# Performance work log

Measured on AMD Instinct MI355X. Metric: run time of the kernel, lower is better.

The kernel has to match this reference:

```python
import jax, jax.numpy as jnp
import numpy as np

H = 512        # hidden_dim
D_IN = 512     # input_dim
N_ACT = 16     # output_dim
DICT = 8192    # dict_len (episodic memory slots)
B = 4096       # batch
N_CYCLES = 10  # LCA iterations
DT_T = 0.6     # LCA dt/tau
EPS = 1e-8     # cosine-similarity eps


def setup_inputs() -> dict:
    key = jax.random.key(0)
    ks = jax.random.split(key, 12)
    NHT = 4 * H + 3  # (N_VSIG+1)*H + N_SSIG
    s = lambda i, shape, sc=1.0: jax.random.normal(ks[i], shape, jnp.float32) * sc
    return {
        "x_t": s(0, (1, B, D_IN)),
        "h_prev": s(1, (1, B, H), 0.1),
        "c_prev": s(2, (1, B, H), 0.1),
        "W_i2h": s(3, (NHT, D_IN), 1.0 / np.sqrt(D_IN)),
        "b_i2h": jnp.zeros((NHT,), jnp.float32),
        "W_h2h": s(4, (NHT, H), 1.0 / np.sqrt(H)),
        "b_h2h": jnp.zeros((NHT,), jnp.float32),
        "vals": s(5, (DICT, H), 0.1),  # episodic memory table
        "W_ih": s(6, (H, H), 1.0 / np.sqrt(H)),
        "b_ih": jnp.zeros((H,), jnp.float32),
        "W_actor": s(7, (N_ACT, H), 1.0 / np.sqrt(H)),
        "b_actor": jnp.zeros((N_ACT,), jnp.float32),
        "W_critic": s(8, (1, H), 1.0 / np.sqrt(H)),
        "b_critic": jnp.zeros((1,), jnp.float32),
        "mem_ptr": 0,
    }


def _lca(sim, leak, comp, w_input):
    # Leaky competing accumulator over memory slots; sim:[B,DICT], scalars:[B,1]
    ff = w_input * sim
    def step(V, _):
        inhib = comp * (jnp.sum(V, axis=-1, keepdims=True) - V)  # lateral inhibition (excl. self)
        V = jax.nn.relu(V + DT_T * (ff - leak * V - inhib))
        return V, None
    V, _ = jax.lax.scan(step, jnp.zeros_like(sim), None, length=N_CYCLES)
    return V


def reference(x_t, h_prev, c_prev, W_i2h, b_i2h, W_h2h, b_h2h, vals,
              W_ih, b_ih, W_actor, b_actor, W_critic, b_critic, mem_ptr):
    x, h, c = x_t[0], h_prev[0], c_prev[0]  # [B, dim]
    preact = x @ W_i2h.T + b_i2h + h @ W_h2h.T + b_h2h  # [B, 4H+3]
    gates = jax.nn.sigmoid(preact[:, :3 * H])
    f_t = gates[:, :H]
    o_t = gates[:, H:2 * H]
    i_t = gates[:, 2 * H:3 * H]
    inps = jax.nn.sigmoid(preact[:, 3 * H + 0])[:, None]  # input strength (gain=1)
    leak = jax.nn.sigmoid(preact[:, 3 * H + 1])[:, None]
    comp = jax.nn.sigmoid(preact[:, 3 * H + 2])[:, None]
    c_new = jnp.tanh(preact[:, 3 * H + 3:])
    c_t = c * f_t + i_t * c_new
    # --- recall: cosine similarity vs memory, then LCA competition ---
    qn = jnp.linalg.norm(c_t, axis=-1, keepdims=True)        # [B,1]
    mn = jnp.linalg.norm(vals, axis=-1, keepdims=True)       # [DICT,1]
    sim = (c_t @ vals.T) / jnp.maximum(qn * mn.T, EPS)       # [B,DICT]
    w = _lca(sim, leak, comp, inps)                          # [B,DICT]
    m_t = w @ vals                                           # [B,H]
    cm_t = c_t + m_t
    # --- encode: ring-buffer scatter write of cm_t into memory ---
    idx = (mem_ptr + jnp.arange(B)) % DICT
    new_vals = vals.at[idx].set(cm_t)
    h_t = o_t * jnp.tanh(cm_t)
    # --- A2C head ---
    a2c_h = jax.nn.relu(h_t @ W_ih.T + b_ih)
    pi = jax.nn.softmax(a2c_h @ W_actor.T + b_actor, axis=-1)
    value = a2c_h @ W_critic.T + b_critic
    return pi, value, h_t, cm_t, m_t, new_vals
```

## Files before the change

kernel.cpp:

```cpp
#include <hip/hip_runtime.h>
#include <hip/hip_fp16.h>
#include <math.h>

#define HH    512
#define DICT  8192
#define BATCH 4096
#define NCYC  10
#define DTT   0.6f

#define BM  128
#define BKT 64

using f16x8 = __attribute__((ext_vector_type(8))) _Float16;
using f32x4 = __attribute__((ext_vector_type(4))) float;

__device__ __forceinline__ float sigmoidf_(float x) { return 1.0f / (1.0f + __expf(-x)); }

__device__ __forceinline__ float waveReduceSum(float v) {
#pragma unroll
  for (int o = 1; o < 64; o <<= 1) v += __shfl_xor(v, o);
  return v;
}

__device__ __forceinline__ void gld16(const void* g, void* l) {
  __builtin_amdgcn_global_load_lds(
      (const __attribute__((address_space(1))) void*)g,
      (__attribute__((address_space(3))) void*)l, 16, 0, 0);
}

template<int N> __device__ __forceinline__ void vmwait() {
  if constexpr (N == 8)      asm volatile("s_waitcnt vmcnt(8)" ::: "memory");
  else if constexpr (N == 6) asm volatile("s_waitcnt vmcnt(6)" ::: "memory");
  else                       asm volatile("s_waitcnt vmcnt(0)" ::: "memory");
  __builtin_amdgcn_sched_barrier(0);
}

__device__ __forceinline__ void blockbar() {
  asm volatile("" ::: "memory");
  __builtin_amdgcn_s_barrier();
  __builtin_amdgcn_sched_barrier(0);
}

template<int ROWS>
__device__ __forceinline__ void stage_tile(const __half* gbase, int ld, char* lds, int tid) {
  constexpr int ISS = ROWS * 8 / 256;
#pragma unroll
  for (int i = 0; i < ISS; ++i) {
    int cidx = i * 256 + tid;
    int row  = cidx >> 3;
    int slot = cidx & 7;
    int k4   = slot ^ (row & 7);
    gld16(gbase + (size_t)row * ld + k4 * 8, lds + cidx * 16);
  }
}

__device__ __forceinline__ f16x8 frag_ld(const char* lds, int row, int kchunk) {
  int slot = kchunk ^ (row & 7);
  return *(const f16x8*)(lds + row * 128 + slot * 16);
}

template<int FN>
__device__ __forceinline__ void tile_mfma(const char* As, const char* Bs,
                                          int lane, int wr, int wc, f32x4 (&acc)[4][FN]) {
  const int g = lane >> 4, r = lane & 15;
#pragma unroll
  for (int ks = 0; ks < 2; ++ks) {
    f16x8 af[4], bfr[FN];
#pragma unroll
    for (int i = 0; i < 4; ++i)
      af[i] = frag_ld(As, wr * 64 + i * 16 + r, ks * 4 + g);
#pragma unroll
    for (int j = 0; j < FN; ++j)
      bfr[j] = frag_ld(Bs, wc * (FN * 16) + j * 16 + r, ks * 4 + g);
#pragma unroll
    for (int i = 0; i < 4; ++i)
#pragma unroll
      for (int j = 0; j < FN; ++j)
        acc[i][j] = __builtin_amdgcn_mfma_f32_16x16x32_f16(af[i], bfr[j], acc[i][j], 0, 0, 0);
  }
}

template<int BN, int FN>
__device__ __forceinline__ void gemm_seg(const __half* A, int lda, const __half* B, int ldb,
                                         int m0, int n0, int K, char* lds, int tid,
                                         f32x4 (&acc)[4][FN]) {
  constexpr int ABYTES = BM * BKT * 2;
  constexpr int BBYTES = BN * BKT * 2;
  constexpr int BUF = ABYTES + BBYTES;
  constexpr int NL = (BM + BN) * 8 / 256;
  const int lane = tid & 63, wid = tid >> 6;
  const int wr = wid >> 1, wc = wid & 1;
  const int nt = K / BKT;
  const __half* Ab = A + (size_t)m0 * lda;
  const __half* Bb = B + (size_t)n0 * ldb;
  stage_tile<BM>(Ab, lda, lds, tid);
  stage_tile<BN>(Bb, ldb, lds + ABYTES, tid);
  int cur = 0;
  for (int t = 0; t < nt; ++t) {
    char* curb = lds + cur * BUF;
    if (t + 1 < nt) {
      char* nxt = lds + (cur ^ 1) * BUF;
      stage_tile<BM>(Ab + (t + 1) * BKT, lda, nxt, tid);
      stage_tile<BN>(Bb + (t + 1) * BKT, ldb, nxt + ABYTES, tid);
      vmwait<NL>();
    } else {
      vmwait<0>();
    }
    blockbar();
    tile_mfma<FN>(curb, curb + ABYTES, lane, wr, wc, acc);
    blockbar();
    cur ^= 1;
  }
}

__device__ __forceinline__ void zero_acc4(f32x4 (&a)[4][4]) {
  f32x4 z = {0.f, 0.f, 0.f, 0.f};
#pragma unroll
  for (int i = 0; i < 4; ++i)
#pragma unroll
    for (int j = 0; j < 4; ++j) a[i][j] = z;
}
__device__ __forceinline__ void zero_acc2(f32x4 (&a)[4][2]) {
  f32x4 z = {0.f, 0.f, 0.f, 0.f};
#pragma unroll
  for (int i = 0; i < 4; ++i)
#pragma unroll
    for (int j = 0; j < 2; ++j) a[i][j] = z;
}

__global__ __launch_bounds__(256) void k_prep(
    const float* __restrict__ x, const float* __restrict__ h,
    const float* __restrict__ Wi, const float* __restrict__ Wh, const float* __restrict__ Wih,
    const float* __restrict__ vals, const int* __restrict__ mptr,
    __half* __restrict__ x_h, __half* __restrict__ h_h,
    __half* __restrict__ Wip_h, __half* __restrict__ Whp_h, __half* __restrict__ Wih_h,
    float* __restrict__ nv, __half* __restrict__ vals_h, float* __restrict__ rmn,
    __half* __restrict__ vT) {
  __shared__ float tile[32][33];
  const int bid = blockIdx.x;
  if (bid < 6400) {
    int gq = bid * 256 + threadIdx.x;
    const float* src; __half* dst; int si, di;
    if (gq < 524288) {
      src = x; dst = x_h; si = di = gq * 4;
    } else if (gq < 1048576) {
      src = h; dst = h_h; si = di = (gq - 524288) * 4;
    } else if (gq < 1310720) {
      int iq = gq - 1048576;
      int jp = iq >> 7, k4 = (iq & 127) << 2;
      int U = jp >> 6, g = (jp >> 4) & 3, r = jp & 15;
      int u = U * 16 + r;
      int orig = g * 512 + u + (g == 3 ? 3 : 0);
      src = Wi; dst = Wip_h; si = orig * 512 + k4; di = jp * 512 + k4;
    } else if (gq < 1572864) {
      int iq = gq - 1310720;
      int jp = iq >> 7, k4 = (iq & 127) << 2;
      int U = jp >> 6, g = (jp >> 4) & 3, r = jp & 15;
      int u = U * 16 + r;
      int orig = g * 512 + u + (g == 3 ? 3 : 0);
      src = Wh; dst = Whp_h; si = orig * 512 + k4; di = jp * 512 + k4;
    } else if (gq < 1638400) {
      int iq = gq - 1572864;
      src = Wih; dst = Wih_h; si = di = iq * 4;
    } else return;
    float4 v = *(const float4*)(src + si);
    *(__half2*)(dst + di)     = __floats2half2_rn(v.x, v.y);
    *(__half2*)(dst + di + 2) = __floats2half2_rn(v.z, v.w);
  } else if (bid < 8448) {
    const int row  = (bid - 6400) * 4 + (threadIdx.x >> 6);
    const int lane = threadIdx.x & 63;
    const float* vr = vals + (size_t)row * HH + lane * 8;
    float4 a = *(const float4*)(vr);
    float4 b = *(const float4*)(vr + 4);
    if (((row + DICT - mptr[0]) & (DICT - 1)) >= BATCH) {
      float* nvp = nv + (size_t)row * HH + lane * 8;
      *(float4*)(nvp)     = a;
      *(float4*)(nvp + 4) = b;
    }
    __half* vh = vals_h + (size_t)row * HH + lane * 8;
    *(__half2*)(vh)     = __floats2half2_rn(a.x, a.y);
    *(__half2*)(vh + 2) = __floats2half2_rn(a.z, a.w);
    *(__half2*)(vh + 4) = __floats2half2_rn(b.x, b.y);
    *(__half2*)(vh + 6) = __floats2half2_rn(b.z, b.w);
    float ss = a.x * a.x + a.y * a.y + a.z * a.z + a.w * a.w
             + b.x * b.x + b.y * b.y + b.z * b.z + b.w * b.w;
    ss = waveReduceSum(ss);
    if (lane == 0) rmn[row] = 1.f / fmaxf(sqrtf(ss), 1e-12f);
  } else {
    const int idx = bid - 8448;
    const int r0 = (idx & 255) * 32, c0 = (idx >> 8) * 32;
    const int tr = threadIdx.x >> 5, tc = threadIdx.x & 31;
#pragma unroll
    for (int p = 0; p < 4; ++p)
      tile[tr + p * 8][tc] = vals[(size_t)(r0 + tr + p * 8) * HH + c0 + tc];
    __syncthreads();
#pragma unroll
    for (int p = 0; p < 4; ++p)
      vT[(size_t)(c0 + tr + p * 8) * DICT + r0 + tc] = __float2half(tile[tc][tr + p * 8]);
  }
}

__global__ __launch_bounds__(256) void k_preact(
    const __half* __restrict__ x_h, const __half* __restrict__ h_h,
    const __half* __restrict__ Wip, const __half* __restrict__ Whp,
    const float* __restrict__ bi, const float* __restrict__ bh,
    const float* __restrict__ c_prev,
    float* __restrict__ ct, float* __restrict__ ot, __half* __restrict__ ct_h) {
  __shared__ char smem[2 * (BM * BKT * 2 + 128 * BKT * 2)] __attribute__((aligned(16)));
  const int tid = threadIdx.x;
  const int m0 = blockIdx.y * 128, n0 = blockIdx.x * 128;
  f32x4 acc[4][4]; zero_acc4(acc);
  gemm_seg<128, 4>(x_h, HH, Wip, HH, m0, n0, HH, smem, tid, acc);
  gemm_seg<128, 4>(h_h, HH, Whp, HH, m0, n0, HH, smem, tid, acc);
  const int lane = tid & 63, wid = tid >> 6, wr = wid >> 1, wc = wid & 1;
  const int r = lane & 15;
  const int u = ((n0 >> 6) + wc) * 16 + r;
  float bsum[4];
#pragma unroll
  for (int g = 0; g < 4; ++g) {
    int orig = g * 512 + u + (g == 3 ? 3 : 0);
    bsum[g] = bi[orig] + bh[orig];
  }
#pragma unroll
  for (int fi = 0; fi < 4; ++fi)
#pragma unroll
    for (int q = 0; q < 4; ++q) {
      int m = m0 + wr * 64 + fi * 16 + (lane >> 4) * 4 + q;
      float f  = sigmoidf_(acc[fi][0][q] + bsum[0]);
      float o  = sigmoidf_(acc[fi][1][q] + bsum[1]);
      float ii = sigmoidf_(acc[fi][2][q] + bsum[2]);
      float cn = tanhf(acc[fi][3][q] + bsum[3]);
      size_t off = (size_t)m * HH + u;
      float cc = c_prev[off] * f + ii * cn;
      ct[off] = cc; ot[off] = o; ct_h[off] = __float2half(cc);
    }
}

__global__ __launch_bounds__(256) void k_scalars(
    const float* __restrict__ x, const float* __restrict__ h,
    const float* __restrict__ Wi, const float* __restrict__ Wh,
    const float* __restrict__ bi, const float* __restrict__ bh,
    const float* __restrict__ ct,
    float* __restrict__ inps, float* __restrict__ leak,
    float* __restrict__ comp, float* __restrict__ rqn) {
  const int b = blockIdx.x, wid = threadIdx.x >> 6, lane = threadIdx.x & 63;
  const int j = lane * 8;
  if (wid < 3) {
    const float* wi = Wi + (size_t)(1536 + wid) * HH + j;
    const float* wh = Wh + (size_t)(1536 + wid) * HH + j;
    const float* xr = x + (size_t)b * HH + j;
    const float* hr = h + (size_t)b * HH + j;
    float4 xa = *(const float4*)(xr), xb = *(const float4*)(xr + 4);
    float4 wa = *(const float4*)(wi), wb = *(const float4*)(wi + 4);
    float4 ha = *(const float4*)(hr), hb = *(const float4*)(hr + 4);
    float4 va = *(const float4*)(wh), vb = *(const float4*)(wh + 4);
    float s = xa.x * wa.x + xa.y * wa.y + xa.z * wa.z + xa.w * wa.w
            + xb.x * wb.x + xb.y * wb.y + xb.z * wb.z + xb.w * wb.w
            + ha.x * va.x + ha.y * va.y + ha.z * va.z + ha.w * va.w
            + hb.x * vb.x + hb.y * vb.y + hb.z * vb.z + hb.w * vb.w;
    s = waveReduceSum(s);
    if (lane == 0) {
      float v = sigmoidf_(s + bi[1536 + wid] + bh[1536 + wid]);
      if (wid == 0) inps[b] = v; else if (wid == 1) leak[b] = v; else comp[b] = v;
    }
  } else {
    const float* cr = ct + (size_t)b * HH + j;
    float4 a = *(const float4*)(cr), d = *(const float4*)(cr + 4);
    float ss = a.x * a.x + a.y * a.y + a.z * a.z + a.w * a.w
             + d.x * d.x + d.y * d.y + d.z * d.z + d.w * d.w;
    ss = waveReduceSum(ss);
    if (lane == 0) rqn[b] = 1.f / fmaxf(sqrtf(ss), 1e-12f);
  }
}

__global__ __launch_bounds__(256) void k_sim(
    const __half* __restrict__ ct_h, const __half* __restrict__ vals_h,
    const float* __restrict__ rqn, const float* __restrict__ rmn,
    __half* __restrict__ sim_h) {
  __shared__ char smem[2 * (BM * BKT * 2 + 128 * BKT * 2)] __attribute__((aligned(16)));
  const int tid = threadIdx.x;
  const int m0 = blockIdx.y * 128, n0 = blockIdx.x * 128;
  f32x4 acc[4][4]; zero_acc4(acc);
  gemm_seg<128, 4>(ct_h, HH, vals_h, HH, m0, n0, HH, smem, tid, acc);
  const int lane = tid & 63, wid = tid >> 6, wr = wid >> 1, wc = wid & 1;
  float* T = (float*)smem;
  const int g = lane >> 4, r = lane & 15;
  const int lrow = tid >> 3, c16 = (tid & 7) * 16;
  const int nR = n0 + c16;
  float rmv[16];
  *(float4*)(rmv)      = *(const float4*)(rmn + nR);
  *(float4*)(rmv + 4)  = *(const float4*)(rmn + nR + 4);
  *(float4*)(rmv + 8)  = *(const float4*)(rmn + nR + 8);
  *(float4*)(rmv + 12) = *(const float4*)(rmn + nR + 12);
#pragma unroll
  for (int fi = 0; fi < 4; ++fi) {
    if (fi) __syncthreads();
#pragma unroll
    for (int fj = 0; fj < 4; ++fj)
#pragma unroll
      for (int q = 0; q < 4; ++q)
        T[(wr * 16 + g * 4 + q) * 132 + wc * 64 + fj * 16 + r] = acc[fi][fj][q];
    __syncthreads();
    int m = m0 + (lrow >> 4) * 64 + fi * 16 + (lrow & 15);
    float rq = rqn[m];
    const float* Tr = T + lrow * 132 + c16;
    f16x8 o0, o1;
#pragma unroll
    for (int j = 0; j < 8; ++j) o0[j] = (_Float16)(Tr[j] * rq * rmv[j]);
#pragma unroll
    for (int j = 0; j < 8; ++j) o1[j] = (_Float16)(Tr[8 + j] * rq * rmv[8 + j]);
    *(f16x8*)(sim_h + (size_t)m * DICT + nR)     = o0;
    *(f16x8*)(sim_h + (size_t)m * DICT + nR + 8) = o1;
  }
}

__global__ __launch_bounds__(256) void k_lca(
    const __half* __restrict__ sim_h, const float* __restrict__ inps,
    const float* __restrict__ leak, const float* __restrict__ comp,
    __half* __restrict__ w_h) {
  const int b = blockIdx.x, t = threadIdx.x;
  const __half* srow = sim_h + (size_t)b * DICT + t * 32;
  const float ffs = DTT * inps[b];
  const float a   = 1.0f - DTT * leak[b] + DTT * comp[b];
  const float cdt = DTT * comp[b];
  float ff[32], V[32];
#pragma unroll
  for (int i = 0; i < 4; ++i) {
    f16x8 v8 = *(const f16x8*)(srow + i * 8);
#pragma unroll
    for (int j = 0; j < 8; ++j) { ff[i * 8 + j] = ffs * (float)v8[j]; V[i * 8 + j] = 0.f; }
  }
  __shared__ float ps[4];
  for (int it = 0; it < NCYC; ++it) {
    float s = 0.f;
#pragma unroll
    for (int i = 0; i < 32; ++i) s += V[i];
    s = waveReduceSum(s);
    if ((t & 63) == 0) ps[t >> 6] = s;
    __syncthreads();
    float S = ps[0] + ps[1] + ps[2] + ps[3];
    __syncthreads();
    float sub = cdt * S;
#pragma unroll
    for (int i = 0; i < 32; ++i) V[i] = fmaxf(fmaf(a, V[i], ff[i] - sub), 0.f);
  }
  __half* wrow = w_h + (size_t)b * DICT + t * 32;
#pragma unroll
  for (int i = 0; i < 4; ++i) {
    f16x8 o8;
#pragma unroll
    for (int j = 0; j < 8; ++j) o8[j] = (_Float16)V[i * 8 + j];
    *(f16x8*)(wrow + i * 8) = o8;
  }
}

__global__ __launch_bounds__(256) void k_mt_p(
    const __half* __restrict__ w_h, const __half* __restrict__ vT_h,
    float* __restrict__ partial) {
  __shared__ char smem[2 * (BM * BKT * 2 + 64 * BKT * 2)] __attribute__((aligned(16)));
  const int tid = threadIdx.x, bid = blockIdx.x;
  const int xcd = bid & 7, idx = bid >> 3;
  const int n = idx & 7, q = idx >> 3;
  const int g = (q << 3) | xcd;
  const int m = g >> 2, s = g & 3;
  const int m0 = m * 128, n0 = n * 64;
  f32x4 acc[4][2]; zero_acc2(acc);
  gemm_seg<64, 2>(w_h + s * 2048, DICT, vT_h + s * 2048, DICT, m0, n0, 2048, smem, tid, acc);
  const int lane = tid & 63, wid = tid >> 6, wr = wid >> 1, wc = wid & 1;
  float* pbase = partial + (size_t)s * (BATCH * HH);
  float* T = (float*)smem;
  const int gg = lane >> 4, r = lane & 15;
  const int lrow = tid >> 3, c8 = (tid & 7) * 8;
#pragma unroll
  for (int fi = 0; fi < 4; ++fi) {
    if (fi) __syncthreads();
#pragma unroll
    for (int fj = 0; fj < 2; ++fj)
#pragma unroll
      for (int qq = 0; qq < 4; ++qq)
        T[(wr * 16 + gg * 4 + qq) * 68 + wc * 32 + fj * 16 + r] = acc[fi][fj][qq];
    __syncthreads();
    int mm = m0 + (lrow >> 4) * 64 + fi * 16 + (lrow & 15);
    float* dst = pbase + (size_t)mm * HH + n0 + c8;
    *(float4*)dst       = *(const float4*)(T + lrow * 68 + c8);
    *(float4*)(dst + 4) = *(const float4*)(T + lrow * 68 + c8 + 4);
  }
}

__global__ __launch_bounds__(256) void k_mt_red(
    const float* __restrict__ partial,
    const float* __restrict__ ct, const float* __restrict__ ot, const int* __restrict__ mptr,
    float* __restrict__ out_mt, float* __restrict__ out_cmt, float* __restrict__ out_ht,
    float* __restrict__ out_nv, __half* __restrict__ ht_h) {
  const int i4 = blockIdx.x * 256 + threadIdx.x;
  const size_t off = (size_t)i4 * 4;
  const int m = i4 >> 7;
  float4 p  = *(const float4*)(partial + off);
  float4 p1 = *(const float4*)(partial + 2097152 + off);
  float4 p2 = *(const float4*)(partial + 4194304 + off);
  float4 p3 = *(const float4*)(partial + 6291456 + off);
  p.x += p1.x + p2.x + p3.x;
  p.y += p1.y + p2.y + p3.y;
  p.z += p1.z + p2.z + p3.z;
  p.w += p1.w + p2.w + p3.w;
  float4 c4 = *(const float4*)(ct + off);
  float4 o4 = *(const float4*)(ot + off);
  float4 cm, hv;
  cm.x = c4.x + p.x; hv.x = o4.x * tanhf(cm.x);
  cm.y = c4.y + p.y; hv.y = o4.y * tanhf(cm.y);
  cm.z = c4.z + p.z; hv.z = o4.z * tanhf(cm.z);
  cm.w = c4.w + p.w; hv.w = o4.w * tanhf(cm.w);
  *(float4*)(out_mt + off)  = p;
  *(float4*)(out_cmt + off) = cm;
  *(float4*)(out_ht + off)  = hv;
  *(__half2*)(ht_h + off)     = __floats2half2_rn(hv.x, hv.y);
  *(__half2*)(ht_h + off + 2) = __floats2half2_rn(hv.z, hv.w);
  const int nvrow = (mptr[0] + m) & (DICT - 1);
  *(float4*)(out_nv + (size_t)nvrow * HH + (off & 511)) = cm;
}

__global__ __launch_bounds__(256) void k_a2c(
    const __half* __restrict__ ht_h, const __half* __restrict__ Wih_h,
    const float* __restrict__ bih, float* __restrict__ a2c) {
  __shared__ char smem[2 * (BM * BKT * 2 + 64 * BKT * 2)] __attribute__((aligned(16)));
  const int tid = threadIdx.x;
  const int bid = blockIdx.x;
  const int xn = (bid >> 3) & 7, ym = (bid & 7) | ((bid >> 6) << 3);
  const int m0 = ym * 128, n0 = xn * 64;
  f32x4 acc[4][2]; zero_acc2(acc);
  gemm_seg<64, 2>(ht_h, HH, Wih_h, HH, m0, n0, HH, smem, tid, acc);
  const int lane = tid & 63, wid = tid >> 6, wr = wid >> 1, wc = wid & 1;
  float* T = (float*)smem;
  const int gg = lane >> 4, r = lane & 15;
  const int lrow = tid >> 3, c8 = (tid & 7) * 8;
  float4 b0 = *(const float4*)(bih + n0 + c8);
  float4 b1 = *(const float4*)(bih + n0 + c8 + 4);
#pragma unroll
  for (int fi = 0; fi < 4; ++fi) {
    if (fi) __syncthreads();
#pragma unroll
    for (int fj = 0; fj < 2; ++fj)
#pragma unroll
      for (int qq = 0; qq < 4; ++qq)
        T[(wr * 16 + gg * 4 + qq) * 68 + wc * 32 + fj * 16 + r] = acc[fi][fj][qq];
    __syncthreads();
    int mm = m0 + (lrow >> 4) * 64 + fi * 16 + (lrow & 15);
    float4 v0 = *(const float4*)(T + lrow * 68 + c8);
    float4 v1 = *(const float4*)(T + lrow * 68 + c8 + 4);
    v0.x = fmaxf(v0.x + b0.x, 0.f); v0.y = fmaxf(v0.y + b0.y, 0.f);
    v0.z = fmaxf(v0.z + b0.z, 0.f); v0.w = fmaxf(v0.w + b0.w, 0.f);
    v1.x = fmaxf(v1.x + b1.x, 0.f); v1.y = fmaxf(v1.y + b1.y, 0.f);
    v1.z = fmaxf(v1.z + b1.z, 0.f); v1.w = fmaxf(v1.w + b1.w, 0.f);
    float* dst = a2c + (size_t)mm * HH + n0 + c8;
    *(float4*)dst       = v0;
    *(float4*)(dst + 4) = v1;
  }
}

__global__ __launch_bounds__(256) void k_actor(
    const float* __restrict__ a2c,
    const float* __restrict__ Wact, const float* __restrict__ bact,
    const float* __restrict__ Wcr, const float* __restrict__ bcr,
    float* __restrict__ out_pi, float* __restrict__ out_val) {
  const int b = blockIdx.x * 4 + (threadIdx.x >> 6);
  const int lane = threadIdx.x & 63;
  const float* hrow = a2c + (size_t)b * HH;
  float4 a0 = *(const float4*)(hrow + (lane << 3));
  float4 a1 = *(const float4*)(hrow + (lane << 3) + 4);
  float lg[17];
#pragma unroll
  for (int o = 0; o < 17; ++o) {
    const float* wr = (o < 16) ? (Wact + (size_t)o * HH) : Wcr;
    float4 w0 = *(const float4*)(wr + (lane << 3));
    float4 w1 = *(const float4*)(wr + (lane << 3) + 4);
    float s = a0.x * w0.x + a0.y * w0.y + a0.z * w0.z + a0.w * w0.w
            + a1.x * w1.x + a1.y * w1.y + a1.z * w1.z + a1.w * w1.w;
    lg[o] = waveReduceSum(s);
  }
#pragma unroll
  for (int o = 0; o < 16; ++o) lg[o] += bact[o];
  float mx = lg[0];
#pragma unroll
  for (int o = 1; o < 16; ++o) mx = fmaxf(mx, lg[o]);
  float e[16], sum = 0.f;
#pragma unroll
  for (int o = 0; o < 16; ++o) { e[o] = __expf(lg[o] - mx); sum += e[o]; }
  float rs = 1.f / sum;
  if (lane == 0) {
#pragma unroll
    for (int o = 0; o < 16; ++o) out_pi[(size_t)b * 16 + o] = e[o] * rs;
    out_val[b] = lg[16] + bcr[0];
  }
}

extern "C" void kernel_launch(void* const* d_in, const int* in_sizes, int n_in,
                              void* d_out, int out_size, void* d_ws, size_t ws_size,
                              hipStream_t stream) {
  const float* x    = (const float*)d_in[0];
  const float* h    = (const float*)d_in[1];
  const float* c    = (const float*)d_in[2];
  const float* Wi   = (const float*)d_in[3];
  const float* bi   = (const float*)d_in[4];
  const float* Wh   = (const float*)d_in[5];
  const float* bh   = (const float*)d_in[6];
  const float* vals = (const float*)d_in[7];
  const float* Wih  = (const float*)d_in[8];
  const float* bih  = (const float*)d_in[9];
  const float* Wact = (const float*)d_in[10];
  const float* bact = (const float*)d_in[11];
  const float* Wcr  = (const float*)d_in[12];
  const float* bcr  = (const float*)d_in[13];
  const int*   mptr = (const int*)d_in[14];

  float* F = (float*)d_ws;
  __half* w_h    = (__half*)F;
  __half* sim_h   = (__half*)(F + 16777216);
  float*  a2c     = F + 16777216;
  float*  partial = F + 33554432;
  float*  ct     = F + 50331648;
  float*  ot     = F + 52428800;
  __half* ct_h   = (__half*)(F + 54525952);
  __half* vals_h = (__half*)(F + 55574528);
  __half* vT_h   = (__half*)(F + 57671680);
  __half* x_h    = (__half*)(F + 59768832);
  __half* ht_h   = x_h;
  __half* h_h    = (__half*)(F + 60817408);
  __half* Wip_h  = (__half*)(F + 61865984);
  __half* Whp_h  = (__half*)(F + 62423040);
  __half* Wih_h  = (__half*)(F + 62980096);
  float*  inps   = F + 63111168;
  float*  leak   = inps + 4096;
  float*  comp   = leak + 4096;
  float*  rqn    = comp + 4096;
  float*  rmn    = rqn + 4096;

  float* out     = (float*)d_out;
  float* out_pi  = out;
  float* out_val = out + 65536;
  float* out_ht  = out + 69632;
  float* out_cmt = out_ht + 2097152;
  float* out_mt  = out_cmt + 2097152;
  float* out_nv  = out_mt + 2097152;

  dim3 b256(256);
  k_prep   <<<12544, b256, 0, stream>>>(x, h, Wi, Wh, Wih, vals, mptr,
                                        x_h, h_h, Wip_h, Whp_h, Wih_h,
                                        out_nv, vals_h, rmn, vT_h);
  k_preact <<<dim3(16, 32), b256, 0, stream>>>(x_h, h_h, Wip_h, Whp_h, bi, bh, c,
                                               ct, ot, ct_h);
  k_scalars<<<BATCH, b256, 0, stream>>>(x, h, Wi, Wh, bi, bh, ct, inps, leak, comp, rqn);
  k_sim    <<<dim3(64, 32), b256, 0, stream>>>(ct_h, vals_h, rqn, rmn, sim_h);
  k_lca    <<<BATCH, b256, 0, stream>>>(sim_h, inps, leak, comp, w_h);
  k_mt_p   <<<1024, b256, 0, stream>>>(w_h, vT_h, partial);
  k_mt_red <<<2048, b256, 0, stream>>>(partial, ct, ot, mptr,
                                       out_mt, out_cmt, out_ht, out_nv, ht_h);
  k_a2c    <<<256, b256, 0, stream>>>(ht_h, Wih_h, bih, a2c);
  k_actor  <<<BATCH / 4, b256, 0, stream>>>(a2c, Wact, bact, Wcr, bcr, out_pi, out_val);
}
```

Baseline: 218.7 us.

## Enlarge sim and mt GEMM tiles with 512-thread blocks and XCD-aware mapping

Rewrites the two large GEMMs (similarity and memory readout) to use 256x256 and 256x128 tiles with 512-thread blocks, K-step 32 using the 16x16x32 f16 MFMA, XOR-swizzled LDS staging and double buffering with finer vmcnt waits. Block indices are remapped so that blocks sharing an A row tile land on the same XCD, for L2 reuse. The aim is higher arithmetic intensity and less redundant global traffic. In exchange the kernels carry more accumulator registers and launch fewer blocks (512 and 256), which risks low occupancy or wave-quantization tail effects.

Measured after the change: 235.9 us. 1.08x slower.

```diff
diff --git a/kernel.cpp b/kernel.cpp
--- a/kernel.cpp
+++ b/kernel.cpp
@@ -31,6 +31,8 @@
 template<int N> __device__ __forceinline__ void vmwait() {
   if constexpr (N == 8)      asm volatile("s_waitcnt vmcnt(8)" ::: "memory");
   else if constexpr (N == 6) asm volatile("s_waitcnt vmcnt(6)" ::: "memory");
+  else if constexpr (N == 4) asm volatile("s_waitcnt vmcnt(4)" ::: "memory");
+  else if constexpr (N == 3) asm volatile("s_waitcnt vmcnt(3)" ::: "memory");
   else                       asm volatile("s_waitcnt vmcnt(0)" ::: "memory");
   __builtin_amdgcn_sched_barrier(0);
 }
@@ -126,6 +128,45 @@
   for (int i = 0; i < 4; ++i)
 #pragma unroll
     for (int j = 0; j < 2; ++j) a[i][j] = z;
+}
+
+__device__ __forceinline__ int swz32(int row, int k) {
+  return k ^ (row & 3) ^ ((row >> 2) & 3);
+}
+
+template<int ROWS, int NT>
+__device__ __forceinline__ void stage32(const __half* gbase, int ld, char* lds, int tid) {
+  constexpr int ISS = ROWS * 4 / NT;
+#pragma unroll
+  for (int i = 0; i < ISS; ++i) {
+    int cidx = i * NT + tid;
+    int row  = cidx >> 2;
+    int slot = cidx & 3;
+    int k4   = swz32(row, slot);
+    gld16(gbase + (size_t)row * ld + k4 * 8, lds + cidx * 16);
+  }
+}
+
+__device__ __forceinline__ f16x8 frag32(const char* lds, int row, int g) {
+  int slot = swz32(row, g);
+  return *(const f16x8*)(lds + row * 64 + slot * 16);
+}
+
+template<int MF, int NF>
+__device__ __forceinline__ void tile_mfma32(const char* As, const char* Bs,
+                                            int arow0, int brow0, int lane,
+                                            f32x4 (&acc)[MF][NF]) {
+  const int g = lane >> 4, r = lane & 15;
+  f16x8 af[MF], bf[NF];
+#pragma unroll
+  for (int i = 0; i < MF; ++i) af[i] = frag32(As, arow0 + i * 16 + r, g);
+#pragma unroll
+  for (int j = 0; j < NF; ++j) bf[j] = frag32(Bs, brow0 + j * 16 + r, g);
+#pragma unroll
+  for (int i = 0; i < MF; ++i)
+#pragma unroll
+    for (int j = 0; j < NF; ++j)
+      acc[i][j] = __builtin_amdgcn_mfma_f32_16x16x32_f16(af[i], bf[j], acc[i][j], 0, 0, 0);
 }
 
 __global__ __launch_bounds__(256) void k_prep(
@@ -273,44 +314,72 @@
   }
 }
 
-__global__ __launch_bounds__(256) void k_sim(
+__global__ __launch_bounds__(512, 2) void k_sim(
     const __half* __restrict__ ct_h, const __half* __restrict__ vals_h,
     const float* __restrict__ rqn, const float* __restrict__ rmn,
     __half* __restrict__ sim_h) {
-  __shared__ char smem[2 * (BM * BKT * 2 + 128 * BKT * 2)] __attribute__((aligned(16)));
-  const int tid = threadIdx.x;
-  const int m0 = blockIdx.y * 128, n0 = blockIdx.x * 128;
-  f32x4 acc[4][4]; zero_acc4(acc);
-  gemm_seg<128, 4>(ct_h, HH, vals_h, HH, m0, n0, HH, smem, tid, acc);
-  const int lane = tid & 63, wid = tid >> 6, wr = wid >> 1, wc = wid & 1;
+  __shared__ char smem[65536] __attribute__((aligned(16)));
+  const int tid = threadIdx.x, lane = tid & 63, wid = tid >> 6;
+  const int wr = wid >> 2, wc = wid & 3;
+  const int bid = blockIdx.x;
+  const int xcd = bid & 7, idx = bid >> 3;
+  const int m0 = (xcd * 2 + (idx & 1)) * 256;
+  const int n0 = (idx >> 1) * 256;
+  f32x4 acc[8][4];
+  { f32x4 z = {0.f, 0.f, 0.f, 0.f};
+#pragma unroll
+    for (int i = 0; i < 8; ++i)
+#pragma unroll
+      for (int j = 0; j < 4; ++j) acc[i][j] = z; }
+  const __half* Ab = ct_h + (size_t)m0 * HH;
+  const __half* Bb = vals_h + (size_t)n0 * HH;
+  stage32<256, 512>(Ab, HH, smem, tid);
+  stage32<256, 512>(Bb, HH, smem + 16384, tid);
+  int cur = 0;
+  for (int t = 0; t < 16; ++t) {
+    char* curb = smem + cur * 32768;
+    if (t < 15) {
+      char* nxt = smem + (cur ^ 1) * 32768;
+      stage32<256, 512>(Ab + (t + 1) * 32, HH, nxt, tid);
+      stage32<256, 512>(Bb + (t + 1) * 32, HH, nxt + 16384, tid);
+      vmwait<4>();
+    } else {
+      vmwait<0>();
+    }
+    blockbar();
+    __builtin_amdgcn_s_setprio(1);
+    tile_mfma32<8, 4>(curb, curb + 16384, wr * 128, wc * 64, lane, acc);
+    __builtin_amdgcn_s_setprio(0);
+    blockbar();
+    cur ^= 1;
+  }
   float* T = (float*)smem;
   const int g = lane >> 4, r = lane & 15;
-  const int lrow = tid >> 3, c16 = (tid & 7) * 16;
-  const int nR = n0 + c16;
+  const int lrow = tid >> 4, seg = (tid & 15) * 16;
   float rmv[16];
-  *(float4*)(rmv)      = *(const float4*)(rmn + nR);
-  *(float4*)(rmv + 4)  = *(const float4*)(rmn + nR + 4);
-  *(float4*)(rmv + 8)  = *(const float4*)(rmn + nR + 8);
-  *(float4*)(rmv + 12) = *(const float4*)(rmn + nR + 12);
-#pragma unroll
-  for (int fi = 0; fi < 4; ++fi) {
+  *(float4*)(rmv)      = *(const float4*)(rmn + n0 + seg);
+  *(float4*)(rmv + 4)  = *(const float4*)(rmn + n0 + seg + 4);
+  *(float4*)(rmv + 8)  = *(const float4*)(rmn + n0 + seg + 8);
+  *(float4*)(rmv + 12) = *(const float4*)(rmn + n0 + seg + 12);
+#pragma unroll
+  for (int fi = 0; fi < 8; ++fi) {
     if (fi) __syncthreads();
 #pragma unroll
     for (int fj = 0; fj < 4; ++fj)
 #pragma unroll
       for (int q = 0; q < 4; ++q)
-        T[(wr * 16 + g * 4 + q) * 132 + wc * 64 + fj * 16 + r] = acc[fi][fj][q];
+        T[(wr * 16 + g * 4 + q) * 260 + wc * 64 + fj * 16 + r] = acc[fi][fj][q];
     __syncthreads();
-    int m = m0 + (lrow >> 4) * 64 + fi * 16 + (lrow & 15);
+    int m = m0 + (lrow >> 4) * 128 + fi * 16 + (lrow & 15);
     float rq = rqn[m];
-    const float* Tr = T + lrow * 132 + c16;
+    const float* Tr = T + lrow * 260 + seg;
     f16x8 o0, o1;
 #pragma unroll
     for (int j = 0; j < 8; ++j) o0[j] = (_Float16)(Tr[j] * rq * rmv[j]);
 #pragma unroll
     for (int j = 0; j < 8; ++j) o1[j] = (_Float16)(Tr[8 + j] * rq * rmv[8 + j]);
-    *(f16x8*)(sim_h + (size_t)m * DICT + nR)     = o0;
-    *(f16x8*)(sim_h + (size_t)m * DICT + nR + 8) = o1;
+    *(f16x8*)(sim_h + (size_t)m * DICT + n0 + seg)     = o0;
+    *(f16x8*)(sim_h + (size_t)m * DICT + n0 + seg + 8) = o1;
   }
 }
 
@@ -354,36 +423,60 @@
   }
 }
 
-__global__ __launch_bounds__(256) void k_mt_p(
+__global__ __launch_bounds__(512, 2) void k_mt_p(
     const __half* __restrict__ w_h, const __half* __restrict__ vT_h,
     float* __restrict__ partial) {
-  __shared__ char smem[2 * (BM * BKT * 2 + 64 * BKT * 2)] __attribute__((aligned(16)));
-  const int tid = threadIdx.x, bid = blockIdx.x;
+  __shared__ char smem[49152] __attribute__((aligned(16)));
+  const int tid = threadIdx.x, lane = tid & 63, wid = tid >> 6;
+  const int wr = wid >> 1, wc = wid & 1;
+  const int bid = blockIdx.x;
   const int xcd = bid & 7, idx = bid >> 3;
-  const int n = idx & 7, q = idx >> 3;
-  const int g = (q << 3) | xcd;
-  const int m = g >> 2, s = g & 3;
-  const int m0 = m * 128, n0 = n * 64;
-  f32x4 acc[4][2]; zero_acc2(acc);
-  gemm_seg<64, 2>(w_h + s * 2048, DICT, vT_h + s * 2048, DICT, m0, n0, 2048, smem, tid, acc);
-  const int lane = tid & 63, wid = tid >> 6, wr = wid >> 1, wc = wid & 1;
+  const int s = xcd >> 1, sub = xcd & 1;
+  const int n = idx >> 3, mq = idx & 7;
+  const int m0 = (mq * 2 + sub) * 256, n0 = n * 128;
+  f32x4 acc[4][4]; zero_acc4(acc);
+  const __half* Ab = w_h + (size_t)m0 * DICT + s * 2048;
+  const __half* Bb = vT_h + (size_t)n0 * DICT + s * 2048;
+  stage32<256, 512>(Ab, DICT, smem, tid);
+  stage32<128, 512>(Bb, DICT, smem + 16384, tid);
+  int cur = 0;
+  for (int t = 0; t < 64; ++t) {
+    char* curb = smem + cur * 24576;
+    if (t < 63) {
+      char* nxt = smem + (cur ^ 1) * 24576;
+      stage32<256, 512>(Ab + (t + 1) * 32, DICT, nxt, tid);
+      stage32<128, 512>(Bb + (t + 1) * 32, DICT, nxt + 16384, tid);
+      vmwait<3>();
+    } else {
+      vmwait<0>();
+    }
+    blockbar();
+    __builtin_amdgcn_s_setprio(1);
+    tile_mfma32<4, 4>(curb, curb + 16384, wr * 64, wc * 64, lane, acc);
+    __builtin_amdgcn_s_setprio(0);
+    blockbar();
+    cur ^= 1;
+  }
+  float* T = (float*)smem;
+  const int g = lane >> 4, r = lane & 15;
+  const int lrow = tid >> 3, seg = (tid & 7) * 16;
   float* pbase = partial + (size_t)s * (BATCH * HH);
-  float* T = (float*)smem;
-  const int gg = lane >> 4, r = lane & 15;
-  const int lrow = tid >> 3, c8 = (tid & 7) * 8;
 #pragma unroll
   for (int fi = 0; fi < 4; ++fi) {
     if (fi) __syncthreads();
 #pragma unroll
-    for (int fj = 0; fj < 2; ++fj)
-#pragma unroll
-      for (int qq = 0; qq < 4; ++qq)
-        T[(wr * 16 + gg * 4 + qq) * 68 + wc * 32 + fj * 16 + r] = acc[fi][fj][qq];
+    for (int fj = 0; fj < 4; ++fj)
+#pragma unroll
+      for (int q = 0; q < 4; ++q)
+        T[(wr * 16 + g * 4 + q) * 132 + wc * 64 + fj * 16 + r] = acc[fi][fj][q];
     __syncthreads();
     int mm = m0 + (lrow >> 4) * 64 + fi * 16 + (lrow & 15);
-    float* dst = pbase + (size_t)mm * HH + n0 + c8;
-    *(float4*)dst       = *(const float4*)(T + lrow * 68 + c8);
-    *(float4*)(dst + 4) = *(const float4*)(T + lrow * 68 + c8 + 4);
+    const float* Tr = T + lrow * 132 + seg;
+    float* dst = pbase + (size_t)mm * HH + n0 + seg;
+    *(float4*)(dst)      = *(const float4*)(Tr);
+    *(float4*)(dst + 4)  = *(const float4*)(Tr + 4);
+    *(float4*)(dst + 8)  = *(const float4*)(Tr + 8);
+    *(float4*)(dst + 12) = *(const float4*)(Tr + 12);
   }
 }
 
@@ -543,15 +636,16 @@
   float* out_nv  = out_mt + 2097152;
 
   dim3 b256(256);
+  dim3 b512(512);
   k_prep   <<<12544, b256, 0, stream>>>(x, h, Wi, Wh, Wih, vals, mptr,
                                         x_h, h_h, Wip_h, Whp_h, Wih_h,
                                         out_nv, vals_h, rmn, vT_h);
   k_preact <<<dim3(16, 32), b256, 0, stream>>>(x_h, h_h, Wip_h, Whp_h, bi, bh, c,
                                                ct, ot, ct_h);
   k_scalars<<<BATCH, b256, 0, stream>>>(x, h, Wi, Wh, bi, bh, ct, inps, leak, comp, rqn);
-  k_sim    <<<dim3(64, 32), b256, 0, stream>>>(ct_h, vals_h, rqn, rmn, sim_h);
+  k_sim    <<<512, b512, 0, stream>>>(ct_h, vals_h, rqn, rmn, sim_h);
   k_lca    <<<BATCH, b256, 0, stream>>>(sim_h, inps, leak, comp, w_h);
-  k_mt_p   <<<1024, b256, 0, stream>>>(w_h, vT_h, partial);
+  k_mt_p   <<<256, b512, 0, stream>>>(w_h, vT_h, partial);
   k_mt_red <<<2048, b256, 0, stream>>>(partial, ct, ot, mptr,
                                        out_mt, out_cmt, out_ht, out_nv, ht_h);
   k_a2c    <<<256, b256, 0, stream>>>(ht_h, Wih_h, bih, a2c);
```
